# Optimization experiments

Hardware: AMD Instinct MI355X
Metric: run time of the kernel (lower is better)

## Reference

```python
import jax, jax.numpy as jnp
import numpy as np

B, T, D, H, LORA = 4, 1024, 1024, 16, 64
HD = D // H
BLOCK_ID, N_BLOCKS = 6, 12


def _ln(x, w, b, eps=1e-5):
    m = x.mean(-1, keepdims=True)
    v = ((x - m) ** 2).mean(-1, keepdims=True)
    return (x - m) * jax.lax.rsqrt(v + eps) * w + b


def _lora(z, a, b, l):
    return l + jnp.tanh(z @ a.T) @ b.T


def setup_inputs() -> dict:
    key = jax.random.key(0)
    ks = iter(jax.random.split(key, 64))
    rn = lambda shape, s: jax.random.normal(next(ks), shape, jnp.float32) * s
    inp = {}
    inp['x'] = rn((B, T, D), 1.0)
    r1 = 1.0 - BLOCK_ID / N_BLOCKS
    i = np.arange(D)
    inp['xw'] = jnp.asarray(1.0 - (i / D) ** r1, jnp.float32)
    for nm in ('rW', 'kW', 'vW', 'gW'):
        inp[nm] = rn((D, D), 0.02)
    for p in ('r', 'k', 'v', 'g', 'd'):
        inp[p + '_la'] = rn((LORA, D), 0.001)
        inp[p + '_lb'] = rn((D, LORA), 0.001)
        inp[p + '_ll'] = rn((D,), 1.0)
    inp['ln_w'] = jnp.full((HD,), ((1 + BLOCK_ID) / N_BLOCKS) ** 0.7, jnp.float32)
    inp['ln_b'] = jnp.zeros((HD,), jnp.float32)
    inp['oW'] = rn((D, D), 0.02)
    inp['init_state'] = rn((H, HD, HD), 1.0)
    r0 = BLOCK_ID / (N_BLOCKS - 1)
    ih = i % HD
    inp['u'] = jnp.asarray(r0 * (1 - ih / (D - 1)) + np.remainder(0.1 * (ih + 1), 3.0), jnp.float32)
    return inp


def reference(x, xw, rW, kW, vW, gW, r_la, r_lb, r_ll, k_la, k_lb, k_ll,
              v_la, v_lb, v_ll, g_la, g_lb, g_ll, d_la, d_lb, d_ll,
              ln_w, ln_b, oW, init_state, u):
    b, t, d = x.shape
    h = init_state.shape[0]
    hd = d // h
    # token shift: xx[t] = x[t-1], xx[0] = 0
    xx = jnp.concatenate([jnp.zeros_like(x[:, :1]), x[:, :-1]], axis=1)
    dx = xx - x
    lerpx = x + dx * xw
    r = (x + dx * _lora(lerpx, r_la, r_lb, r_ll)) @ rW.T
    k = (x + dx * _lora(lerpx, k_la, k_lb, k_ll)) @ kW.T
    v = (x + dx * _lora(lerpx, v_la, v_lb, v_ll)) @ vW.T
    g = (x + dx * _lora(lerpx, g_la, g_lb, g_ll)) @ gW.T
    w = jnp.exp(-jnp.exp(_lora(x + dx * _lora(lerpx, d_la, d_lb, d_ll), d_la, d_lb, d_ll)))
    # [B,T,D] -> [T,B,H,hd] for the time scan
    split = lambda z: z.reshape(b, t, h, hd).transpose(1, 0, 2, 3)
    rs, ws, ks, vs = split(r), split(w), split(k), split(v)
    uh = u.reshape(h, hd)
    st0 = jnp.broadcast_to(init_state, (b, h, hd, hd))

    def step(st, inp):
        rt, wt, kt, vt = inp
        kv = jnp.einsum('bhi,bhj->bhij', kt, vt)      # outer product
        y = jnp.einsum('bhi,bhij->bhj', rt, st + uh[None, :, :, None] * kv)
        return wt[..., None] * st + kv, y             # diag(w) @ S + kv

    st1, ys = jax.lax.scan(step, st0, (rs, ws, ks, vs))  # ys: [T,B,H,hd]
    o = jax.nn.silu(g.reshape(b, t, h, hd)) * _ln(ys.transpose(1, 0, 2, 3), ln_w, ln_b)
    return o.reshape(b, t, d) @ oW.T, st1
```

## Files before the change

kernel.cpp:

```cpp
#include <hip/hip_runtime.h>
#include <hip/hip_bf16.h>

typedef unsigned short u16;
typedef unsigned int u32;
typedef __attribute__((ext_vector_type(2))) float f32x2;
typedef __attribute__((ext_vector_type(4))) float f32x4;
typedef __attribute__((ext_vector_type(8))) short s16x8;

#define AS1 __attribute__((address_space(1)))
#define AS3 __attribute__((address_space(3)))

#define NB 4
#define TTOK 1024
#define DD 1024
#define NH 16
#define HD 64
#define MT 4096
#define NCH 16
#define CLEN 64

static __device__ __forceinline__ float b2f(u16 u) {
  union { unsigned int u; float f; } c; c.u = ((unsigned int)u) << 16; return c.f;
}
static __device__ __forceinline__ u16 f2b(float f) {
  union { float f; unsigned int u; } c; c.f = f;
  return (u16)((c.u + 0x7fffu + ((c.u >> 16) & 1u)) >> 16);
}
static __device__ __forceinline__ void gload16(const u16* g, u16* l) {
  __builtin_amdgcn_global_load_lds((const AS1 u32*)g, (AS3 u32*)l, 16, 0, 0);
}
static __device__ __forceinline__ int swz(int lin) {
  return lin ^ (((lin >> 9) & 3) << 5) ^ (((lin >> 7) & 1) << 4);
}

__global__ __launch_bounds__(256) void convW(const float* __restrict__ s0, const float* __restrict__ s1,
                                             const float* __restrict__ s2, const float* __restrict__ s3,
                                             const float* __restrict__ s4, u16* __restrict__ dst) {
  long f = ((long)blockIdx.x * 256 + threadIdx.x) << 2;
  int sel = (int)(f >> 20);
  const float* s = sel == 0 ? s0 : sel == 1 ? s1 : sel == 2 ? s2 : sel == 3 ? s3 : s4;
  long off = f & 1048575;
  f32x4 v = *(const f32x4*)&s[off];
  ushort4 o; o.x = f2b(v[0]); o.y = f2b(v[1]); o.z = f2b(v[2]); o.w = f2b(v[3]);
  *(ushort4*)&dst[f] = o;
}

__global__ __launch_bounds__(256) void convLora(
    const float* a0, const float* a1, const float* a2, const float* a3, const float* a4,
    const float* b0, const float* b1, const float* b2, const float* b3, const float* b4,
    const float* l0, const float* l1, const float* l2, const float* l3, const float* l4,
    u16* __restrict__ laD, u16* __restrict__ lbD, float* __restrict__ llD) {
  long f = ((long)blockIdx.x * 256 + threadIdx.x) << 2;
  if (f < 327680) {
    int sel = (int)(f >> 16); long off = f & 65535;
    const float* s = sel == 0 ? a0 : sel == 1 ? a1 : sel == 2 ? a2 : sel == 3 ? a3 : a4;
    f32x4 v = *(const f32x4*)&s[off];
    ushort4 o; o.x = f2b(v[0]); o.y = f2b(v[1]); o.z = f2b(v[2]); o.w = f2b(v[3]);
    *(ushort4*)&laD[f] = o;
  } else if (f < 655360) {
    long g = f - 327680;
    int sel = (int)(g >> 16); long off = g & 65535;
    const float* s = sel == 0 ? b0 : sel == 1 ? b1 : sel == 2 ? b2 : sel == 3 ? b3 : b4;
    f32x4 v = *(const f32x4*)&s[off];
    ushort4 o; o.x = f2b(v[0]); o.y = f2b(v[1]); o.z = f2b(v[2]); o.w = f2b(v[3]);
    *(ushort4*)&lbD[g] = o;
  } else if (f < 660480) {
    long g = f - 655360;
    int sel = (int)(g >> 10); long off = g & 1023;
    const float* s = sel == 0 ? l0 : sel == 1 ? l1 : sel == 2 ? l2 : sel == 3 ? l3 : l4;
    *(f32x4*)&llD[g] = *(const f32x4*)&s[off];
  }
}

__global__ __launch_bounds__(256) void prep(const float* __restrict__ x, const float* __restrict__ xw,
                                            u16* __restrict__ lerpx, u16* __restrict__ xB,
                                            u16* __restrict__ dxB) {
  long f = ((long)blockIdx.x * 256 + threadIdx.x) << 2;
  int d = (int)(f & (DD - 1));
  int m = (int)(f >> 10);
  int t = m & (TTOK - 1);
  f32x4 xv = *(const f32x4*)&x[f];
  f32x4 xm = {};
  if (t > 0) xm = *(const f32x4*)&x[f - DD];
  f32x4 xwv = *(const f32x4*)&xw[d];
  f32x4 dx = xm - xv;
  f32x4 lp = xv + dx * xwv;
  ushort4 o; o.x = f2b(lp[0]); o.y = f2b(lp[1]); o.z = f2b(lp[2]); o.w = f2b(lp[3]);
  *(ushort4*)&lerpx[f] = o;
  ushort4 ox; ox.x = f2b(xv[0]); ox.y = f2b(xv[1]); ox.z = f2b(xv[2]); ox.w = f2b(xv[3]);
  *(ushort4*)&xB[f] = ox;
  ushort4 od; od.x = f2b(dx[0]); od.y = f2b(dx[1]); od.z = f2b(dx[2]); od.w = f2b(dx[3]);
  *(ushort4*)&dxB[f] = od;
}

template<int BM, int BN, int EPI>
__launch_bounds__(256)
__global__ void gemm2(const u16* __restrict__ Ab, long sAz,
                      const u16* __restrict__ Bb, long sBz,
                      void* __restrict__ Ob, long sOz,
                      const float* __restrict__ llb,
                      const u16* __restrict__ xB,
                      const u16* __restrict__ dxB,
                      int M, int N, int K) {
  __shared__ __align__(16) u16 As[BM * 64];
  __shared__ __align__(16) u16 Bs[BN * 64];
  const int z = blockIdx.z;
  const u16* A = Ab + (long)z * sAz;
  const u16* Bw = Bb + (long)z * sBz;
  const int m0 = blockIdx.x * BM;
  const int n0 = blockIdx.y * BN;
  const int tid = threadIdx.x;
  const int l = tid & 63;
  const int wv = tid >> 6;
  constexpr int WM = BM / 2, WN = BN / 2;
  constexpr int FM = WM / 16, FN = WN / 16;
  const int wm0 = (wv >> 1) * WM, wn0 = (wv & 1) * WN;
  const int lrow = l & 15, lk = (l >> 4) * 8;
  constexpr int GA = BM / 32, GB = BN / 32;
  int gA[GA], gB[GB];
#pragma unroll
  for (int q = 0; q < GA; ++q) {
    int d = (q * 256 + tid) * 16;
    int bb = swz(d);
    gA[q] = (m0 + (bb >> 7)) * K + ((bb & 127) >> 1);
  }
#pragma unroll
  for (int q = 0; q < GB; ++q) {
    int d = (q * 256 + tid) * 16;
    int bb = swz(d);
    gB[q] = (n0 + (bb >> 7)) * K + ((bb & 127) >> 1);
  }
  int aOff[FM][2], bOff[FN][2];
#pragma unroll
  for (int m = 0; m < FM; ++m)
#pragma unroll
    for (int kk = 0; kk < 2; ++kk)
      aOff[m][kk] = swz(((wm0 + m * 16 + lrow) << 7) + (kk << 6) + (lk << 1));
#pragma unroll
  for (int n = 0; n < FN; ++n)
#pragma unroll
    for (int kk = 0; kk < 2; ++kk)
      bOff[n][kk] = swz(((wn0 + n * 16 + lrow) << 7) + (kk << 6) + (lk << 1));
  f32x4 acc[FM][FN] = {};
  for (int k0 = 0; k0 < K; k0 += 64) {
    __syncthreads();
#pragma unroll
    for (int q = 0; q < GA; ++q)
      gload16(&A[(long)gA[q] + k0], (u16*)((char*)As + (q * 256 + tid) * 16));
#pragma unroll
    for (int q = 0; q < GB; ++q)
      gload16(&Bw[(long)gB[q] + k0], (u16*)((char*)Bs + (q * 256 + tid) * 16));
    __syncthreads();
#pragma unroll
    for (int kk = 0; kk < 2; ++kk) {
      s16x8 af[FM], bfr[FN];
#pragma unroll
      for (int m = 0; m < FM; ++m) af[m] = *(const s16x8*)((const char*)As + aOff[m][kk]);
#pragma unroll
      for (int n = 0; n < FN; ++n) bfr[n] = *(const s16x8*)((const char*)Bs + bOff[n][kk]);
#pragma unroll
      for (int m = 0; m < FM; ++m)
#pragma unroll
        for (int n = 0; n < FN; ++n)
          acc[m][n] = __builtin_amdgcn_mfma_f32_16x16x32_bf16(af[m], bfr[n], acc[m][n], 0, 0, 0);
    }
  }
#pragma unroll
  for (int m = 0; m < FM; ++m) {
#pragma unroll
    for (int n = 0; n < FN; ++n) {
      const int j = n0 + wn0 + n * 16 + lrow;
#pragma unroll
      for (int q = 0; q < 4; ++q) {
        const int i = m0 + wm0 + m * 16 + (l >> 4) * 4 + q;
        const long off = (long)i * N + j;
        float v = acc[m][n][q];
        if constexpr (EPI == 0) {
          ((float*)Ob + (long)z * sOz)[off] = v;
        } else if constexpr (EPI == 1) {
          ((u16*)Ob + (long)z * sOz)[off] = f2b(tanhf(v));
        } else if constexpr (EPI == 2) {
          float val = b2f(xB[off]) + b2f(dxB[off]) * (llb[(long)z * N + j] + v);
          ((u16*)Ob + (long)z * sOz)[off] = f2b(val);
        } else if constexpr (EPI == 3) {
          ((float*)Ob + (long)z * sOz)[off] = expf(-expf(llb[j] + v));
        } else {
          ((u16*)Ob + (long)z * sOz)[off] = f2b(v);
        }
      }
    }
  }
}

__global__ __launch_bounds__(512) void scan_local(
    const u16* __restrict__ rP, const u16* __restrict__ kP,
    const u16* __restrict__ vP, const float* __restrict__ wP,
    const float* __restrict__ uP, u16* __restrict__ ysB,
    u16* __restrict__ rtil, float* __restrict__ SL, float* __restrict__ AC) {
  __shared__ __align__(16) float Rf[64 * 64];
  __shared__ __align__(16) float Kf[64 * 64];
  __shared__ __align__(16) float Wf[64 * 64];
  __shared__ __align__(16) float Ys[64 * 64];
  __shared__ __align__(16) u16 Vs[64 * 64];
  __shared__ __align__(16) u16 Rt[64 * 64];
  const int bhc = blockIdx.x;
  const int c = bhc & (NCH - 1), h = (bhc >> 4) & (NH - 1), b = bhc >> 8;
  const int tid = threadIdx.x;
  const int l = tid & 63;
  const int qu = tid >> 6;
  const int g = l >> 3;
  const int j = qu * 8 + (l & 7);
  const long base0 = ((long)(b * TTOK + c * CLEN) << 10) + h * HD;
  const int st = tid >> 3, sjo = (tid & 7) * 8;
  gload16(&vP[base0 + (long)st * DD + sjo], (u16*)Vs + tid * 8);
#pragma unroll
  for (int q = 0; q < 2; ++q) {
    int cidx = q * 512 + tid;
    int t = cidx >> 4, off = (cidx & 15) * 4;
    __builtin_amdgcn_global_load_lds((const AS1 u32*)&wP[base0 + (long)t * DD + off],
                                     (AS3 u32*)((float*)Wf + cidx * 4), 16, 0, 0);
  }
  {
    s16x8 rv = *(const s16x8*)&rP[base0 + (long)st * DD + sjo];
    s16x8 kv = *(const s16x8*)&kP[base0 + (long)st * DD + sjo];
    f32x4 r0, r1, k0, k1;
#pragma unroll
    for (int e = 0; e < 4; ++e) {
      r0[e] = b2f((u16)rv[e]); r1[e] = b2f((u16)rv[e + 4]);
      k0[e] = b2f((u16)kv[e]); k1[e] = b2f((u16)kv[e + 4]);
    }
    *(f32x4*)&Rf[st * 64 + sjo] = r0; *(f32x4*)&Rf[st * 64 + sjo + 4] = r1;
    *(f32x4*)&Kf[st * 64 + sjo] = k0; *(f32x4*)&Kf[st * 64 + sjo + 4] = k1;
  }
  __syncthreads();
  f32x2 u2[4];
#pragma unroll
  for (int e = 0; e < 4; ++e) u2[e] = *(const f32x2*)&uP[h * HD + 8 * g + 2 * e];
  f32x2 s2[4] = {};
  float Aj = 1.f;
  for (int tt = 0; tt < CLEN; ++tt) {
    const int ro = tt * 64 + 8 * g;
    const f32x4 r03 = *(const f32x4*)&Rf[ro];
    const f32x4 r47 = *(const f32x4*)&Rf[ro + 4];
    const f32x4 k03 = *(const f32x4*)&Kf[ro];
    const f32x4 k47 = *(const f32x4*)&Kf[ro + 4];
    const f32x4 w03 = *(const f32x4*)&Wf[ro];
    const f32x4 w47 = *(const f32x4*)&Wf[ro + 4];
    const float vj = b2f(Vs[tt * 64 + j]);
    const f32x2 vj2 = {vj, vj};
    f32x2 y2 = {0.f, 0.f};
    {
      const f32x2 rp = {r03[0], r03[1]}, kp = {k03[0], k03[1]}, wp = {w03[0], w03[1]};
      const f32x2 uk = u2[0] * kp;
      y2 = __builtin_elementwise_fma(rp, __builtin_elementwise_fma(uk, vj2, s2[0]), y2);
      s2[0] = __builtin_elementwise_fma(wp, s2[0], kp * vj2);
    }
    {
      const f32x2 rp = {r03[2], r03[3]}, kp = {k03[2], k03[3]}, wp = {w03[2], w03[3]};
      const f32x2 uk = u2[1] * kp;
      y2 = __builtin_elementwise_fma(rp, __builtin_elementwise_fma(uk, vj2, s2[1]), y2);
      s2[1] = __builtin_elementwise_fma(wp, s2[1], kp * vj2);
    }
    {
      const f32x2 rp = {r47[0], r47[1]}, kp = {k47[0], k47[1]}, wp = {w47[0], w47[1]};
      const f32x2 uk = u2[2] * kp;
      y2 = __builtin_elementwise_fma(rp, __builtin_elementwise_fma(uk, vj2, s2[2]), y2);
      s2[2] = __builtin_elementwise_fma(wp, s2[2], kp * vj2);
    }
    {
      const f32x2 rp = {r47[2], r47[3]}, kp = {k47[2], k47[3]}, wp = {w47[2], w47[3]};
      const f32x2 uk = u2[3] * kp;
      y2 = __builtin_elementwise_fma(rp, __builtin_elementwise_fma(uk, vj2, s2[3]), y2);
      s2[3] = __builtin_elementwise_fma(wp, s2[3], kp * vj2);
    }
    float y = y2[0] + y2[1];
    y += __shfl_xor(y, 8, 64);
    y += __shfl_xor(y, 16, 64);
    y += __shfl_xor(y, 32, 64);
    if ((l & 56) == 0) {
      const float rj = Rf[tt * 64 + j];
      Rt[tt * 64 + j] = f2b(rj * Aj);
      Aj *= Wf[tt * 64 + j];
      Ys[tt * 64 + j] = y;
    }
  }
#pragma unroll
  for (int e = 0; e < 4; ++e) {
    SL[((long)bhc * 64 + 8 * g + 2 * e) * 64 + j] = s2[e][0];
    SL[((long)bhc * 64 + 8 * g + 2 * e + 1) * 64 + j] = s2[e][1];
  }
  if ((l & 56) == 0) AC[(long)bhc * 64 + j] = Aj;
  __syncthreads();
  {
    const f32x4 a = *(const f32x4*)&Ys[st * 64 + sjo];
    const f32x4 bq = *(const f32x4*)&Ys[st * 64 + sjo + 4];
    s16x8 o;
#pragma unroll
    for (int e = 0; e < 4; ++e) { o[e] = (short)f2b(a[e]); o[e + 4] = (short)f2b(bq[e]); }
    *(s16x8*)&ysB[base0 + (long)st * DD + sjo] = o;
    *(s16x8*)&rtil[base0 + (long)st * DD + sjo] = *(const s16x8*)&Rt[st * 64 + sjo];
  }
}

__global__ __launch_bounds__(256) void scan_prop(
    float* __restrict__ SL, const float* __restrict__ AC,
    const float* __restrict__ initS, float* __restrict__ st1) {
  const int bh = blockIdx.x >> 2;
  const int jq = blockIdx.x & 3;
  const int h = bh & (NH - 1);
  const int i = threadIdx.x >> 2;
  const int jo = jq * 16 + (threadIdx.x & 3) * 4;
  f32x4 sin4 = *(const f32x4*)(initS + ((long)h * 64 + i) * 64 + jo);
  for (int cc = 0; cc < NCH; ++cc) {
    const long bhc = (long)bh * NCH + cc;
    f32x4* slp = (f32x4*)(SL + (bhc * 64 + i) * 64 + jo);
    const float Ai = AC[bhc * 64 + i];
    f32x4 sl = *slp;
    *slp = sin4;
    sin4 = Ai * sin4 + sl;
  }
  *(f32x4*)(st1 + ((long)bh * 64 + i) * 64 + jo) = sin4;
}

__global__ __launch_bounds__(256) void scan_corr(
    const float* __restrict__ SL, const u16* __restrict__ rtil, float* __restrict__ ysC) {
  __shared__ __align__(16) float S[64 * 64];
  const int bhc = blockIdx.x;
  const int c = bhc & (NCH - 1), h = (bhc >> 4) & (NH - 1), b = bhc >> 8;
  const int tid = threadIdx.x;
  const f32x4* sp = (const f32x4*)(SL + (long)bhc * 4096);
  for (int q = tid; q < 1024; q += 256) ((f32x4*)S)[q] = sp[q];
  __syncthreads();
  const int t = tid >> 2, jg = (tid & 3) * 16;
  const long base = ((long)(b * TTOK + c * CLEN + t) * DD) + h * HD;
  f32x4 yacc[4] = {};
  const u16* rp = rtil + base;
#pragma unroll 8
  for (int i = 0; i < 64; ++i) {
    const float r = b2f(rp[i]);
    const f32x4* srow = (const f32x4*)&S[i * 64 + jg];
#pragma unroll
    for (int e = 0; e < 4; ++e) yacc[e] += r * srow[e];
  }
  f32x4* yp = (f32x4*)(ysC + base + jg);
#pragma unroll
  for (int e = 0; e < 4; ++e) yp[e] = yacc[e];
}

__global__ __launch_bounds__(256) void ln_silu(
    const u16* __restrict__ ysB, const float* __restrict__ ysC,
    const u16* __restrict__ gP,
    const float* __restrict__ lnw, const float* __restrict__ lnb,
    u16* __restrict__ oB) {
  const int ridx = blockIdx.x * 4 + (threadIdx.x >> 6);
  const int lane = threadIdx.x & 63;
  const long basem = (long)ridx * 64;
  const float y = b2f(ysB[basem + lane]) + ysC[basem + lane];
  float su = y, sq = y * y;
#pragma unroll
  for (int msk = 1; msk < 64; msk <<= 1) {
    su += __shfl_xor(su, msk, 64);
    sq += __shfl_xor(sq, msk, 64);
  }
  const float mean = su * (1.f / 64.f);
  const float var = sq * (1.f / 64.f) - mean * mean;
  const float rs = rsqrtf(var + 1e-5f);
  const float g = b2f(gP[basem + lane]);
  const float silu = g / (1.f + expf(-g));
  const float val = silu * ((y - mean) * rs * lnw[lane] + lnb[lane]);
  oB[basem + lane] = f2b(val);
}

extern "C" void kernel_launch(void* const* d_in, const int* in_sizes, int n_in,
                              void* d_out, int out_size, void* d_ws, size_t ws_size,
                              hipStream_t stream) {
  const float* x   = (const float*)d_in[0];
  const float* xw  = (const float*)d_in[1];
  const float* rW  = (const float*)d_in[2];
  const float* kW  = (const float*)d_in[3];
  const float* vW  = (const float*)d_in[4];
  const float* gW  = (const float*)d_in[5];
  const float* r_la = (const float*)d_in[6],  *r_lb = (const float*)d_in[7],  *r_ll = (const float*)d_in[8];
  const float* k_la = (const float*)d_in[9],  *k_lb = (const float*)d_in[10], *k_ll = (const float*)d_in[11];
  const float* v_la = (const float*)d_in[12], *v_lb = (const float*)d_in[13], *v_ll = (const float*)d_in[14];
  const float* g_la = (const float*)d_in[15], *g_lb = (const float*)d_in[16], *g_ll = (const float*)d_in[17];
  const float* d_la = (const float*)d_in[18], *d_lb = (const float*)d_in[19], *d_ll = (const float*)d_in[20];
  const float* lnw = (const float*)d_in[21];
  const float* lnb = (const float*)d_in[22];
  const float* oW  = (const float*)d_in[23];
  const float* initS = (const float*)d_in[24];
  const float* uP  = (const float*)d_in[25];
  float* out = (float*)d_out;

  char* ws = (char*)d_ws;
  u16*   W_all  = (u16*)(ws + 0);
  u16*   la_all = (u16*)(ws + 10485760);
  u16*   lb_all = (u16*)(ws + 11141120);
  float* ll_all = (float*)(ws + 11796480);
  u16*   lerpx  = (u16*)(ws + 11816960);
  u16*   xB     = (u16*)(ws + 20205568);
  u16*   dxB    = (u16*)(ws + 28594176);
  u16*   t1_all = (u16*)(ws + 36982784);
  u16*   z_all  = (u16*)(ws + 39604224);
  u16*   rkvg   = (u16*)(ws + 81547264);
  float* wbuf   = (float*)(ws + 115101696);
  u16*   rtil   = (u16*)(ws + 131878912);
  float* SL     = (float*)(ws + 140267520);
  float* AC     = (float*)(ws + 157044736);
  u16*   ysB    = (u16*)(ws + 157306880);
  u16*   oB     = (u16*)(ws + 174084096);
  float* ysC    = (float*)(ws + 115101696);

  convW<<<5120, 256, 0, stream>>>(rW, kW, vW, gW, oW, W_all);
  convLora<<<645, 256, 0, stream>>>(r_la, k_la, v_la, g_la, d_la,
                                    r_lb, k_lb, v_lb, g_lb, d_lb,
                                    r_ll, k_ll, v_ll, g_ll, d_ll,
                                    la_all, lb_all, ll_all);
  prep<<<4096, 256, 0, stream>>>(x, xw, lerpx, xB, dxB);

  gemm2<64, 64, 1><<<dim3(64, 1, 5), 256, 0, stream>>>(
      lerpx, 0L, la_all, 65536L, (void*)t1_all, 262144L, nullptr, nullptr, nullptr, MT, 64, 1024);
  gemm2<128, 128, 2><<<dim3(32, 8, 5), 256, 0, stream>>>(
      t1_all, 262144L, lb_all, 65536L, (void*)z_all, 4194304L, ll_all, xB, dxB, MT, 1024, 64);
  gemm2<64, 64, 1><<<dim3(64, 1, 1), 256, 0, stream>>>(
      z_all + 4L * 4194304, 0L, la_all + 4L * 65536, 0L, (void*)t1_all, 0L, nullptr, nullptr, nullptr, MT, 64, 1024);
  gemm2<128, 128, 3><<<dim3(32, 8, 1), 256, 0, stream>>>(
      t1_all, 0L, lb_all + 4L * 65536, 0L, (void*)wbuf, 0L, ll_all + 4096, nullptr, nullptr, MT, 1024, 64);
  gemm2<128, 128, 4><<<dim3(32, 8, 4), 256, 0, stream>>>(
      z_all, 4194304L, W_all, 1048576L, (void*)rkvg, 4194304L, nullptr, nullptr, nullptr, MT, 1024, 1024);

  scan_local<<<1024, 512, 0, stream>>>(rkvg, rkvg + 4194304L, rkvg + 2L * 4194304, wbuf,
                                       uP, ysB, rtil, SL, AC);
  scan_prop<<<256, 256, 0, stream>>>(SL, AC, initS, out + 4194304);
  scan_corr<<<1024, 256, 0, stream>>>(SL, rtil, ysC);

  ln_silu<<<16384, 256, 0, stream>>>(ysB, ysC, rkvg + 3L * 4194304, lnw, lnb, oB);
  gemm2<128, 128, 0><<<dim3(32, 8, 1), 256, 0, stream>>>(
      oB, 0L, W_all + 4L * 1048576, 0L, (void*)out, 0L, nullptr, nullptr, nullptr, MT, 1024, 1024);
}
```

Measured before the change: 357.5 us.

## Remap scan_local so each wave owns state rows and reduce y through LDS

Changes the thread mapping in the chunk-local scan: each wave now owns an 8-row slice of the state for all 64 value columns, instead of each wave holding 8 columns across all rows. The per-token cross-lane shuffle reduction is replaced by buffering 8 tokens of partial sums per wave in shared memory and reducing them across waves once per 8-token group, with results written directly to global memory. It also folds u*k*v into a single kv product. This removes three shuffles per token but adds two block barriers per 8 tokens and LDS traffic for the partial sums.

```diff
diff --git a/kernel.cpp b/kernel.cpp
--- a/kernel.cpp
+++ b/kernel.cpp
@@ -200,16 +200,14 @@
   __shared__ __align__(16) float Rf[64 * 64];
   __shared__ __align__(16) float Kf[64 * 64];
   __shared__ __align__(16) float Wf[64 * 64];
-  __shared__ __align__(16) float Ys[64 * 64];
+  __shared__ __align__(16) float Y8[8][8][64];
   __shared__ __align__(16) u16 Vs[64 * 64];
   __shared__ __align__(16) u16 Rt[64 * 64];
   const int bhc = blockIdx.x;
   const int c = bhc & (NCH - 1), h = (bhc >> 4) & (NH - 1), b = bhc >> 8;
   const int tid = threadIdx.x;
   const int l = tid & 63;
-  const int qu = tid >> 6;
-  const int g = l >> 3;
-  const int j = qu * 8 + (l & 7);
+  const int wv = tid >> 6;
   const long base0 = ((long)(b * TTOK + c * CLEN) << 10) + h * HD;
   const int st = tid >> 3, sjo = (tid & 7) * 8;
   gload16(&vP[base0 + (long)st * DD + sjo], (u16*)Vs + tid * 8);
@@ -235,71 +233,74 @@
   __syncthreads();
   f32x2 u2[4];
 #pragma unroll
-  for (int e = 0; e < 4; ++e) u2[e] = *(const f32x2*)&uP[h * HD + 8 * g + 2 * e];
+  for (int e = 0; e < 4; ++e) u2[e] = *(const f32x2*)&uP[h * HD + 8 * wv + 2 * e];
   f32x2 s2[4] = {};
   float Aj = 1.f;
-  for (int tt = 0; tt < CLEN; ++tt) {
-    const int ro = tt * 64 + 8 * g;
-    const f32x4 r03 = *(const f32x4*)&Rf[ro];
-    const f32x4 r47 = *(const f32x4*)&Rf[ro + 4];
-    const f32x4 k03 = *(const f32x4*)&Kf[ro];
-    const f32x4 k47 = *(const f32x4*)&Kf[ro + 4];
-    const f32x4 w03 = *(const f32x4*)&Wf[ro];
-    const f32x4 w47 = *(const f32x4*)&Wf[ro + 4];
-    const float vj = b2f(Vs[tt * 64 + j]);
-    const f32x2 vj2 = {vj, vj};
-    f32x2 y2 = {0.f, 0.f};
+  for (int t0 = 0; t0 < CLEN; t0 += 8) {
+    float y8[8];
+#pragma unroll
+    for (int q = 0; q < 8; ++q) {
+      const int tt = t0 + q;
+      const int ro = tt * 64 + 8 * wv;
+      const f32x4 rA = *(const f32x4*)&Rf[ro];
+      const f32x4 rB = *(const f32x4*)&Rf[ro + 4];
+      const f32x4 kA = *(const f32x4*)&Kf[ro];
+      const f32x4 kB = *(const f32x4*)&Kf[ro + 4];
+      const f32x4 wA = *(const f32x4*)&Wf[ro];
+      const f32x4 wB = *(const f32x4*)&Wf[ro + 4];
+      const float vj = b2f(Vs[tt * 64 + l]);
+      const f32x2 vj2 = {vj, vj};
+      f32x2 y2 = {0.f, 0.f};
+      {
+        const f32x2 rp = {rA[0], rA[1]}, kp = {kA[0], kA[1]}, wp = {wA[0], wA[1]};
+        const f32x2 kv = kp * vj2;
+        y2 = __builtin_elementwise_fma(rp, __builtin_elementwise_fma(u2[0], kv, s2[0]), y2);
+        s2[0] = __builtin_elementwise_fma(wp, s2[0], kv);
+      }
+      {
+        const f32x2 rp = {rA[2], rA[3]}, kp = {kA[2], kA[3]}, wp = {wA[2], wA[3]};
+        const f32x2 kv = kp * vj2;
+        y2 = __builtin_elementwise_fma(rp, __builtin_elementwise_fma(u2[1], kv, s2[1]), y2);
+        s2[1] = __builtin_elementwise_fma(wp, s2[1], kv);
+      }
+      {
+        const f32x2 rp = {rB[0], rB[1]}, kp = {kB[0], kB[1]}, wp = {wB[0], wB[1]};
+        const f32x2 kv = kp * vj2;
+        y2 = __builtin_elementwise_fma(rp, __builtin_elementwise_fma(u2[2], kv, s2[2]), y2);
+        s2[2] = __builtin_elementwise_fma(wp, s2[2], kv);
+      }
+      {
+        const f32x2 rp = {rB[2], rB[3]}, kp = {kB[2], kB[3]}, wp = {wB[2], wB[3]};
+        const f32x2 kv = kp * vj2;
+        y2 = __builtin_elementwise_fma(rp, __builtin_elementwise_fma(u2[3], kv, s2[3]), y2);
+        s2[3] = __builtin_elementwise_fma(wp, s2[3], kv);
+      }
+      y8[q] = y2[0] + y2[1];
+      if (wv == 0) {
+        const float rj = Rf[tt * 64 + l];
+        Rt[tt * 64 + l] = f2b(rj * Aj);
+        Aj *= Wf[tt * 64 + l];
+      }
+    }
+#pragma unroll
+    for (int q = 0; q < 8; ++q) Y8[wv][q][l] = y8[q];
+    __syncthreads();
     {
-      const f32x2 rp = {r03[0], r03[1]}, kp = {k03[0], k03[1]}, wp = {w03[0], w03[1]};
-      const f32x2 uk = u2[0] * kp;
-      y2 = __builtin_elementwise_fma(rp, __builtin_elementwise_fma(uk, vj2, s2[0]), y2);
-      s2[0] = __builtin_elementwise_fma(wp, s2[0], kp * vj2);
+      float acc = Y8[0][wv][l];
+#pragma unroll
+      for (int w2 = 1; w2 < 8; ++w2) acc += Y8[w2][wv][l];
+      ysB[base0 + (long)(t0 + wv) * DD + l] = f2b(acc);
     }
-    {
-      const f32x2 rp = {r03[2], r03[3]}, kp = {k03[2], k03[3]}, wp = {w03[2], w03[3]};
-      const f32x2 uk = u2[1] * kp;
-      y2 = __builtin_elementwise_fma(rp, __builtin_elementwise_fma(uk, vj2, s2[1]), y2);
-      s2[1] = __builtin_elementwise_fma(wp, s2[1], kp * vj2);
-    }
-    {
-      const f32x2 rp = {r47[0], r47[1]}, kp = {k47[0], k47[1]}, wp = {w47[0], w47[1]};
-      const f32x2 uk = u2[2] * kp;
-      y2 = __builtin_elementwise_fma(rp, __builtin_elementwise_fma(uk, vj2, s2[2]), y2);
-      s2[2] = __builtin_elementwise_fma(wp, s2[2], kp * vj2);
-    }
-    {
-      const f32x2 rp = {r47[2], r47[3]}, kp = {k47[2], k47[3]}, wp = {w47[2], w47[3]};
-      const f32x2 uk = u2[3] * kp;
-      y2 = __builtin_elementwise_fma(rp, __builtin_elementwise_fma(uk, vj2, s2[3]), y2);
-      s2[3] = __builtin_elementwise_fma(wp, s2[3], kp * vj2);
-    }
-    float y = y2[0] + y2[1];
-    y += __shfl_xor(y, 8, 64);
-    y += __shfl_xor(y, 16, 64);
-    y += __shfl_xor(y, 32, 64);
-    if ((l & 56) == 0) {
-      const float rj = Rf[tt * 64 + j];
-      Rt[tt * 64 + j] = f2b(rj * Aj);
-      Aj *= Wf[tt * 64 + j];
-      Ys[tt * 64 + j] = y;
-    }
+    __syncthreads();
   }
 #pragma unroll
   for (int e = 0; e < 4; ++e) {
-    SL[((long)bhc * 64 + 8 * g + 2 * e) * 64 + j] = s2[e][0];
-    SL[((long)bhc * 64 + 8 * g + 2 * e + 1) * 64 + j] = s2[e][1];
-  }
-  if ((l & 56) == 0) AC[(long)bhc * 64 + j] = Aj;
+    SL[((long)bhc * 64 + 8 * wv + 2 * e) * 64 + l] = s2[e][0];
+    SL[((long)bhc * 64 + 8 * wv + 2 * e + 1) * 64 + l] = s2[e][1];
+  }
+  if (wv == 0) AC[(long)bhc * 64 + l] = Aj;
   __syncthreads();
-  {
-    const f32x4 a = *(const f32x4*)&Ys[st * 64 + sjo];
-    const f32x4 bq = *(const f32x4*)&Ys[st * 64 + sjo + 4];
-    s16x8 o;
-#pragma unroll
-    for (int e = 0; e < 4; ++e) { o[e] = (short)f2b(a[e]); o[e + 4] = (short)f2b(bq[e]); }
-    *(s16x8*)&ysB[base0 + (long)st * DD + sjo] = o;
-    *(s16x8*)&rtil[base0 + (long)st * DD + sjo] = *(const s16x8*)&Rt[st * 64 + sjo];
-  }
+  *(s16x8*)&rtil[base0 + (long)st * DD + sjo] = *(const s16x8*)&Rt[st * 64 + sjo];
 }
 
 __global__ __launch_bounds__(256) void scan_prop(
```

Result: no change. 355.0 us (-0.7%).
